# Kernel tuning notes

Hardware: AMD Instinct MI355X
Metric: run time of the kernel (lower is better)

The kernel has to match this reference:

```python
import jax, jax.numpy as jnp
import numpy as np

BS, IN_DIM, OUT_DIM, N_MASKS = 512, 784, 1024, 16


def setup_inputs() -> dict:
    key = jax.random.key(0)
    k_x, k_s, k_m, k_k, k_b = jax.random.split(key, 5)
    x = jax.random.normal(k_x, (BS, IN_DIM), dtype=jnp.float32)
    state = jax.random.randint(k_s, (BS, 1), 0, N_MASKS, dtype=jnp.int32)
    # binary connectivity masks, one per ordering/state (MADE-style)
    masks = jax.random.bernoulli(k_m, 0.5, (N_MASKS, IN_DIM, OUT_DIM)).astype(jnp.float32)
    # RandomNormal(mean=0, stddev=0.1) initializers from build()
    kernel = 0.1 * jax.random.normal(k_k, (IN_DIM, OUT_DIM), dtype=jnp.float32)
    b_0 = 0.1 * jax.random.normal(k_b, (1, OUT_DIM), dtype=jnp.float32)
    return {"x": x, "state": state, "masks": masks, "kernel": kernel, "b_0": b_0}


def reference(x, state, masks, kernel, b_0):
    # gather per-sample mask: [bs, in_dim, out_dim]
    m = masks[state.reshape(-1)]
    # out[b,o] = sum_i x[b,i] * kernel[i,o] * m[b,i,o]  (masked per-sample matmul)
    out = jnp.einsum('bi,io,bio->bo', x, kernel, m) + b_0
    return jax.nn.relu(out)
```

## Files before the change

kernel.cpp:

```cpp
#include <hip/hip_runtime.h>
#include <hip/hip_bf16.h>


#define IN_DIM 784
#define OUT_DIM 1024
#define BS 512

typedef __attribute__((ext_vector_type(8))) short bf16x8;
typedef __attribute__((ext_vector_type(16))) float f32x16;

#define XT_OFF 0u
#define KQ_OFF (1u << 20)
#define MB_OFF (3u << 20)

#define NBITS_BLOCKS 6656
#define NKERN_BLOCKS 416
#define NXT_BLOCKS   392

static __device__ inline short f2bf(float f) {
    __hip_bfloat16 h = __float2bfloat16(f);
    short r; __builtin_memcpy(&r, &h, 2); return r;
}

__global__ __launch_bounds__(256) void made_pre(
    const float* __restrict__ x,
    const float* __restrict__ masks,
    const float* __restrict__ kern,
    unsigned char* __restrict__ ws)
{
    const int bid = blockIdx.x, tid = threadIdx.x;
    const int lane = tid & 63;
    const int q    = tid >> 6;
    const int l31  = lane & 31, khl = lane >> 5;
    const int stp  = q ? 12 : 13;
    const int qoff = q ? (16 + 192 * q) : 0;

    if (bid < NBITS_BLOCKS) {
        const int s  = bid / 416;
        const int r  = bid % 416;
        const int ot = r / 13;
        const int t  = r % 13;
        unsigned b = 0;
        if (t < stp) {
            const int kb = qoff + t * 16 + khl * 8;
            const float* mrow = masks + ((size_t)s * IN_DIM + kb) * OUT_DIM + ot * 32 + l31;
#pragma unroll
            for (int e = 0; e < 8; ++e)
                b |= (mrow[e * OUT_DIM] != 0.f ? 1u : 0u) << e;
        }
        ws[MB_OFF + ((((size_t)(s * 32 + ot) * 4 + q) * 13 + t) * 64 + lane)] =
            (unsigned char)b;
    } else if (bid < NBITS_BLOCKS + NKERN_BLOCKS) {
        const int r  = bid - NBITS_BLOCKS;
        const int ot = r / 13;
        const int t  = r % 13;
        bf16x8 kv;
#pragma unroll
        for (int e = 0; e < 8; ++e) kv[e] = 0;
        if (t < stp) {
            const int kb = qoff + t * 16 + khl * 8;
            const float* krow = kern + (size_t)kb * OUT_DIM + ot * 32 + l31;
#pragma unroll
            for (int e = 0; e < 8; ++e) kv[e] = f2bf(krow[e * OUT_DIM]);
        }
        *(bf16x8*)(ws + KQ_OFF + (((size_t)(ot * 4 + q) * 13 + t) * 64 + lane) * 16) = kv;
    } else {
        const int i = (bid - NBITS_BLOCKS - NKERN_BLOCKS) * 256 + tid;
        float4 v = ((const float4*)x)[i];
        ushort4 o;
        o.x = (unsigned short)f2bf(v.x);
        o.y = (unsigned short)f2bf(v.y);
        o.z = (unsigned short)f2bf(v.z);
        o.w = (unsigned short)f2bf(v.w);
        ((ushort4*)(ws + XT_OFF))[i] = o;
    }
}

__global__ __launch_bounds__(512, 4) void made_main(
    const int*           __restrict__ state,
    const unsigned char* __restrict__ ws,
    const float*         __restrict__ bias,
    float*               __restrict__ out)
{
    __shared__ int   list[BS];
    __shared__ int   cnt;
    __shared__ float red[3][2][16][64];

    const int tid  = threadIdx.x;
    const int lane = tid & 63;
    const int w    = tid >> 6;
    const int q    = w & 3;
    const int m    = w >> 2;
    const int s    = blockIdx.x & 15;
    const int ot   = blockIdx.x >> 4;

    if (tid == 0) cnt = 0;
    __syncthreads();
    { int st = state[tid]; if (st == s) { int p = atomicAdd(&cnt, 1); list[p] = tid; } }
    __syncthreads();
    const int ns = cnt;
    if (ns == 0) return;

    const int l31 = lane & 31, khl = lane >> 5;
    const int qoff = q ? (16 + 192 * q) : 0;

    int ridx = m * 32 + l31; if (ridx >= ns) ridx = ns - 1;
    const unsigned short* xrow =
        (const unsigned short*)(ws + XT_OFF) + (size_t)list[ridx] * IN_DIM;
    bf16x8 a[13];
#pragma unroll
    for (int t = 0; t < 13; ++t) {
        const int off = (q && t == 12) ? qoff : qoff + t * 16;
        a[t] = *(const bf16x8*)(xrow + off + khl * 8);
    }

    const uint4* kp = (const uint4*)(ws + KQ_OFF) + ((size_t)(ot * 4 + q) * 13) * 64 + lane;
    const unsigned char* bp = ws + MB_OFF + (((size_t)(s * 32 + ot) * 4 + q) * 13) * 64 + lane;

    f32x16 acc;
#pragma unroll
    for (int r = 0; r < 16; ++r) acc[r] = 0.f;

#pragma unroll
    for (int t = 0; t < 13; ++t) {
        uint4 kv = kp[t * 64];
        unsigned bb = bp[t * 64];
        uint4 bv;
        bv.x = kv.x & ((bb &   1u ? 0xFFFFu : 0u) | (bb &   2u ? 0xFFFF0000u : 0u));
        bv.y = kv.y & ((bb &   4u ? 0xFFFFu : 0u) | (bb &   8u ? 0xFFFF0000u : 0u));
        bv.z = kv.z & ((bb &  16u ? 0xFFFFu : 0u) | (bb &  32u ? 0xFFFF0000u : 0u));
        bv.w = kv.w & ((bb &  64u ? 0xFFFFu : 0u) | (bb & 128u ? 0xFFFF0000u : 0u));
        bf16x8 bfr; __builtin_memcpy(&bfr, &bv, 16);
        acc = __builtin_amdgcn_mfma_f32_32x32x16_bf16(a[t], bfr, acc, 0, 0, 0);
    }

    if (q) {
#pragma unroll
        for (int j = 0; j < 16; ++j) red[q - 1][m][j][lane] = acc[j];
    }
    __syncthreads();
    if (q == 0) {
        const float bv = bias[ot * 32 + l31];
#pragma unroll
        for (int j = 0; j < 16; ++j) {
            float v = acc[j] + red[0][m][j][lane] + red[1][m][j][lane] + red[2][m][j][lane];
            const int row = (j & 3) + 8 * (j >> 2) + 4 * khl;
            const int sr  = m * 32 + row;
            if (sr < ns) {
                float o = v + bv;
                out[(size_t)list[sr] * OUT_DIM + ot * 32 + l31] = o > 0.f ? o : 0.f;
            }
        }
    }
}

extern "C" void kernel_launch(void* const* d_in, const int* in_sizes, int n_in,
                              void* d_out, int out_size, void* d_ws, size_t ws_size,
                              hipStream_t stream) {
    (void)in_sizes; (void)n_in; (void)out_size; (void)ws_size;
    const float* x     = (const float*)d_in[0];
    const int*   state = (const int*)  d_in[1];
    const float* masks = (const float*)d_in[2];
    const float* kern  = (const float*)d_in[3];
    const float* b0    = (const float*)d_in[4];
    float* out = (float*)d_out;
    unsigned char* ws = (unsigned char*)d_ws;

    made_pre<<<dim3(NBITS_BLOCKS + NKERN_BLOCKS + NXT_BLOCKS), dim3(256), 0, stream>>>(
        x, masks, kern, ws);
    made_main<<<dim3(512), dim3(512), 0, stream>>>(state, ws, b0, out);
}
```

Before: 26.24 us.

## Coalesce mask and kernel preprocessing with float4 row reads and bit transposes

Restructures the preprocessing kernel so each block reads 16 full rows of the mask or kernel with coalesced float4 loads, instead of strided per-lane column reads spread over thousands of small blocks. Bits and bf16 values are transposed in registers into the MFMA-fragment layout and written as 32-bit words and uint4 slots. A separate set of blocks zeroes the padding tiles that were previously written inline. This cuts the block count and the uncoalesced global traffic on the 51MB mask read, at the cost of more register work per thread and scattered 4-byte stores.

```diff
diff --git a/kernel.cpp b/kernel.cpp
--- a/kernel.cpp
+++ b/kernel.cpp
@@ -13,59 +13,86 @@
 #define KQ_OFF (1u << 20)
 #define MB_OFF (3u << 20)
 
-#define NBITS_BLOCKS 6656
-#define NKERN_BLOCKS 416
+#define NMASK_BLOCKS 784
+#define NKERN_BLOCKS 49
 #define NXT_BLOCKS   392
+#define NPAD_BLOCKS  96
 
 static __device__ inline short f2bf(float f) {
     __hip_bfloat16 h = __float2bfloat16(f);
     short r; __builtin_memcpy(&r, &h, 2); return r;
 }
 
-__global__ __launch_bounds__(256) void made_pre(
+static __device__ inline void c_to_qt(int c, int& q, int& t) {
+    if (c < 13) { q = 0; t = c; }
+    else        { q = 1 + (c - 13) / 12; t = (c - 13) % 12; }
+}
+
+__global__ __launch_bounds__(256) void made_pre7(
     const float* __restrict__ x,
     const float* __restrict__ masks,
     const float* __restrict__ kern,
     unsigned char* __restrict__ ws)
 {
     const int bid = blockIdx.x, tid = threadIdx.x;
-    const int lane = tid & 63;
-    const int q    = tid >> 6;
-    const int l31  = lane & 31, khl = lane >> 5;
-    const int stp  = q ? 12 : 13;
-    const int qoff = q ? (16 + 192 * q) : 0;
-
-    if (bid < NBITS_BLOCKS) {
-        const int s  = bid / 416;
-        const int r  = bid % 416;
-        const int ot = r / 13;
-        const int t  = r % 13;
-        unsigned b = 0;
-        if (t < stp) {
-            const int kb = qoff + t * 16 + khl * 8;
-            const float* mrow = masks + ((size_t)s * IN_DIM + kb) * OUT_DIM + ot * 32 + l31;
-#pragma unroll
-            for (int e = 0; e < 8; ++e)
-                b |= (mrow[e * OUT_DIM] != 0.f ? 1u : 0u) << e;
-        }
-        ws[MB_OFF + ((((size_t)(s * 32 + ot) * 4 + q) * 13 + t) * 64 + lane)] =
-            (unsigned char)b;
-    } else if (bid < NBITS_BLOCKS + NKERN_BLOCKS) {
-        const int r  = bid - NBITS_BLOCKS;
-        const int ot = r / 13;
-        const int t  = r % 13;
-        bf16x8 kv;
-#pragma unroll
-        for (int e = 0; e < 8; ++e) kv[e] = 0;
-        if (t < stp) {
-            const int kb = qoff + t * 16 + khl * 8;
-            const float* krow = kern + (size_t)kb * OUT_DIM + ot * 32 + l31;
-#pragma unroll
-            for (int e = 0; e < 8; ++e) kv[e] = f2bf(krow[e * OUT_DIM]);
-        }
-        *(bf16x8*)(ws + KQ_OFF + (((size_t)(ot * 4 + q) * 13 + t) * 64 + lane) * 16) = kv;
-    } else {
-        const int i = (bid - NBITS_BLOCKS - NKERN_BLOCKS) * 256 + tid;
+
+    if (bid < NMASK_BLOCKS) {
+        const int s = bid / 49, c = bid % 49;
+        const float4* mrow =
+            (const float4*)(masks + ((size_t)s * IN_DIM + c * 16) * OUT_DIM) + tid;
+        unsigned nib[16];
+#pragma unroll
+        for (int r = 0; r < 16; ++r) {
+            float4 v = mrow[r * 256];
+            nib[r] = (v.x != 0.f ? 1u : 0u) | (v.y != 0.f ? 2u : 0u)
+                   | (v.z != 0.f ? 4u : 0u) | (v.w != 0.f ? 8u : 0u);
+        }
+        int q, t; c_to_qt(c, q, t);
+        const int ot = tid >> 3;
+        const size_t base32 =
+            ((((size_t)(s * 32 + ot) * 4 + q) * 13 + t) * 16);
+        unsigned* mb = (unsigned*)(ws + MB_OFF);
+#pragma unroll
+        for (int khl = 0; khl < 2; ++khl) {
+            unsigned wd = 0;
+#pragma unroll
+            for (int j = 0; j < 4; ++j) {
+                unsigned by = 0;
+#pragma unroll
+                for (int e = 0; e < 8; ++e)
+                    by |= ((nib[khl * 8 + e] >> j) & 1u) << e;
+                wd |= by << (8 * j);
+            }
+            mb[base32 + khl * 8 + (tid & 7)] = wd;
+        }
+    } else if (bid < NMASK_BLOCKS + NKERN_BLOCKS) {
+        const int c = bid - NMASK_BLOCKS;
+        const float4* krow = (const float4*)(kern + (size_t)c * 16 * OUT_DIM) + tid;
+        unsigned short ku[16][4];
+#pragma unroll
+        for (int r = 0; r < 16; ++r) {
+            float4 v = krow[r * 256];
+            ku[r][0] = (unsigned short)f2bf(v.x);
+            ku[r][1] = (unsigned short)f2bf(v.y);
+            ku[r][2] = (unsigned short)f2bf(v.z);
+            ku[r][3] = (unsigned short)f2bf(v.w);
+        }
+        int q, t; c_to_qt(c, q, t);
+        const int ot = tid >> 3;
+        uint4* kq = (uint4*)(ws + KQ_OFF) + ((size_t)(ot * 4 + q) * 13 + t) * 64;
+#pragma unroll
+        for (int khl = 0; khl < 2; ++khl)
+#pragma unroll
+            for (int j = 0; j < 4; ++j) {
+                uint4 slot;
+                slot.x = (unsigned)ku[khl*8+0][j] | ((unsigned)ku[khl*8+1][j] << 16);
+                slot.y = (unsigned)ku[khl*8+2][j] | ((unsigned)ku[khl*8+3][j] << 16);
+                slot.z = (unsigned)ku[khl*8+4][j] | ((unsigned)ku[khl*8+5][j] << 16);
+                slot.w = (unsigned)ku[khl*8+6][j] | ((unsigned)ku[khl*8+7][j] << 16);
+                kq[khl * 32 + (tid & 7) * 4 + j] = slot;
+            }
+    } else if (bid < NMASK_BLOCKS + NKERN_BLOCKS + NXT_BLOCKS) {
+        const int i = (bid - NMASK_BLOCKS - NKERN_BLOCKS) * 256 + tid;
         float4 v = ((const float4*)x)[i];
         ushort4 o;
         o.x = (unsigned short)f2bf(v.x);
@@ -73,10 +100,15 @@
         o.z = (unsigned short)f2bf(v.z);
         o.w = (unsigned short)f2bf(v.w);
         ((ushort4*)(ws + XT_OFF))[i] = o;
-    }
-}
-
-__global__ __launch_bounds__(512, 4) void made_main(
+    } else {
+        const int g   = (bid - NMASK_BLOCKS - NKERN_BLOCKS - NXT_BLOCKS) * 256 + tid;
+        const int run = g >> 4, off = g & 15;
+        const int sot = run / 3, q = run % 3 + 1;
+        ((unsigned*)(ws + MB_OFF))[((size_t)(sot * 4 + q) * 13 + 12) * 16 + off] = 0u;
+    }
+}
+
+__global__ __launch_bounds__(512, 4) void made_main7(
     const int*           __restrict__ state,
     const unsigned char* __restrict__ ws,
     const float*         __restrict__ bias,
@@ -166,7 +198,7 @@
     float* out = (float*)d_out;
     unsigned char* ws = (unsigned char*)d_ws;
 
-    made_pre<<<dim3(NBITS_BLOCKS + NKERN_BLOCKS + NXT_BLOCKS), dim3(256), 0, stream>>>(
-        x, masks, kern, ws);
-    made_main<<<dim3(512), dim3(512), 0, stream>>>(state, ws, b0, out);
-}
+    made_pre7<<<dim3(NMASK_BLOCKS + NKERN_BLOCKS + NXT_BLOCKS + NPAD_BLOCKS),
+                dim3(256), 0, stream>>>(x, masks, kern, ws);
+    made_main7<<<dim3(512), dim3(512), 0, stream>>>(state, ws, b0, out);
+}
```

Result: no change. 26.25 us (+0.1%).
